# Kernel tuning notes

Measured on AMD Instinct MI355X. Metric: run time of the kernel, lower is better.

The kernel has to match this reference:

```python
import jax, jax.numpy as jnp
import numpy as np

N = 50000
E = 800000


def _segment_softmax(logits, seg, n):
    m = jax.ops.segment_max(logits, seg, num_segments=n)
    e = jnp.exp(logits - m[seg])
    s = jax.ops.segment_sum(e, seg, num_segments=n)
    return e / (s[seg] + 1e-16)


def _gin_layer(x, src, dst, w1, b1, w2, b2, n):
    # GINConv, eps=0: mlp(x + sum_{j->i} x_j); MLP = Linear-ReLU-Linear
    agg = jax.ops.segment_sum(x[src], dst, num_segments=n)
    h = x + agg
    h = jnp.maximum(h @ w1 + b1, 0.0)
    return h @ w2 + b2


def _gat_layer(x, src, dst, w, a_src, a_dst, b, n):
    # GATConv heads=1, add_self_loops=True, leaky_relu slope 0.2
    src = jnp.concatenate([src, jnp.arange(n, dtype=src.dtype)])
    dst = jnp.concatenate([dst, jnp.arange(n, dtype=dst.dtype)])
    h = x @ w                                  # [N, D]
    alpha_s = h @ a_src                        # [N]
    alpha_d = h @ a_dst                        # [N]
    logits = jax.nn.leaky_relu(alpha_s[src] + alpha_d[dst], negative_slope=0.2)
    alpha = _segment_softmax(logits, dst, n)   # [E+N]
    out = jax.ops.segment_sum(h[src] * alpha[:, None], dst, num_segments=n)
    return out + b


def setup_inputs() -> dict:
    key = jax.random.key(0)
    ks = jax.random.split(key, 24)

    def w(k, shape, fan_in):
        return (jax.random.normal(k, shape, dtype=jnp.float32) * (1.0 / np.sqrt(fan_in))).astype(jnp.float32)

    inp = {
        "x": jax.random.normal(ks[0], (N, 10), dtype=jnp.float32),
        "edge_index": jax.random.randint(ks[1], (2, E), 0, N, dtype=jnp.int64 if jax.config.jax_enable_x64 else jnp.int32),
        "edge_attr": jax.random.normal(ks[2], (E, 3), dtype=jnp.float32),
        # GIN layer 1: MLP([10, 64, 64])
        "gin1_w1": w(ks[3], (10, 64), 10), "gin1_b1": jnp.zeros((64,), jnp.float32),
        "gin1_w2": w(ks[4], (64, 64), 64), "gin1_b2": jnp.zeros((64,), jnp.float32),
        # GIN layer 2: MLP([64, 128, 128])
        "gin2_w1": w(ks[5], (64, 128), 64), "gin2_b1": jnp.zeros((128,), jnp.float32),
        "gin2_w2": w(ks[6], (128, 128), 128), "gin2_b2": jnp.zeros((128,), jnp.float32),
        # GAT layer 1: 128 -> 256, heads=1
        "gat1_w": w(ks[7], (128, 256), 128),
        "gat1_asrc": w(ks[8], (256,), 256), "gat1_adst": w(ks[9], (256,), 256),
        "gat1_b": jnp.zeros((256,), jnp.float32),
        # GAT layer 2: 256 -> 128, heads=1, concat=False
        "gat2_w": w(ks[10], (256, 128), 256),
        "gat2_asrc": w(ks[11], (128,), 128), "gat2_adst": w(ks[12], (128,), 128),
        "gat2_b": jnp.zeros((128,), jnp.float32),
    }
    return inp


def reference(x, edge_index, edge_attr,
              gin1_w1, gin1_b1, gin1_w2, gin1_b2,
              gin2_w1, gin2_b1, gin2_w2, gin2_b2,
              gat1_w, gat1_asrc, gat1_adst, gat1_b,
              gat2_w, gat2_asrc, gat2_adst, gat2_b):
    src, dst = edge_index[0], edge_index[1]
    n = x.shape[0]
    # edge_attr is accepted but ignored (GINConv does not consume edge features)
    h = _gin_layer(x, src, dst, gin1_w1, gin1_b1, gin1_w2, gin1_b2, n)
    h = jnp.maximum(h, 0.0)
    h = _gin_layer(h, src, dst, gin2_w1, gin2_b1, gin2_w2, gin2_b2, n)
    h = _gat_layer(h, src, dst, gat1_w, gat1_asrc, gat1_adst, gat1_b, n)
    h = jnp.maximum(h, 0.0)
    h = _gat_layer(h, src, dst, gat2_w, gat2_asrc, gat2_adst, gat2_b, n)
    return h
```

## Files before the change

kernel.cpp:

```cpp
#include <hip/hip_runtime.h>
#include <math.h>

__device__ __forceinline__ float lrelu(float x){ return x > 0.f ? x : 0.2f*x; }

typedef short s16x8 __attribute__((ext_vector_type(8)));
typedef float f32x4 __attribute__((ext_vector_type(4)));
typedef unsigned short u16x8 __attribute__((ext_vector_type(8)));

__device__ __forceinline__ f32x4 bmma(s16x8 a, s16x8 b, f32x4 c){
  return __builtin_amdgcn_mfma_f32_16x16x32_bf16(a, b, c, 0, 0, 0);
}

__device__ __forceinline__ unsigned short f2bf(float f){
  unsigned u = __float_as_uint(f);
  unsigned r = (u + 0x7fffu + ((u >> 16) & 1u)) >> 16;
  return (unsigned short)r;
}
__device__ __forceinline__ float bf2f(unsigned short h){
  return __uint_as_float(((unsigned)h) << 16);
}

__global__ void k_deg(const int* __restrict__ dst, int* __restrict__ deg, int E){
  int e = blockIdx.x*blockDim.x + threadIdx.x;
  if(e < E) atomicAdd(&deg[dst[e]], 1);
}

__global__ __launch_bounds__(1024) void k_scan1(const int* __restrict__ deg,
                                                int* __restrict__ part,
                                                int* __restrict__ bsum, int n){
  int i = blockIdx.x*1024 + threadIdx.x;
  int lane = threadIdx.x & 63, wv = threadIdx.x >> 6;
  int v = (i < n) ? deg[i] : 0;
  int s = v;
  #pragma unroll
  for(int off=1; off<64; off<<=1){
    int t = __shfl_up(s, off);
    if(lane >= off) s += t;
  }
  __shared__ int wsum[16];
  if(lane==63) wsum[wv] = s;
  __syncthreads();
  if(wv==0 && lane<16){
    int t = wsum[lane], ss = t;
    #pragma unroll
    for(int off=1; off<16; off<<=1){
      int u = __shfl_up(ss, off);
      if(lane >= off) ss += u;
    }
    wsum[lane] = ss - t;
    if(lane==15) bsum[blockIdx.x] = ss;
  }
  __syncthreads();
  if(i < n) part[i] = s - v + wsum[wv];
}

__global__ __launch_bounds__(1024) void k_scan2(int* __restrict__ bsum, int nb){
  int i = threadIdx.x;
  int lane = i & 63, wv = i >> 6;
  int v = (i < nb) ? bsum[i] : 0;
  int s = v;
  #pragma unroll
  for(int off=1; off<64; off<<=1){
    int t = __shfl_up(s, off);
    if(lane >= off) s += t;
  }
  __shared__ int wsum[16];
  if(lane==63) wsum[wv] = s;
  __syncthreads();
  if(wv==0 && lane<16){
    int t = wsum[lane], ss = t;
    #pragma unroll
    for(int off=1; off<16; off<<=1){
      int u = __shfl_up(ss, off);
      if(lane >= off) ss += u;
    }
    wsum[lane] = ss - t;
  }
  __syncthreads();
  if(i < nb) bsum[i] = s - v + wsum[wv];
}

__global__ void k_scan3(const int* __restrict__ part, const int* __restrict__ bsum,
                        int* __restrict__ offs, int n, int E){
  int i = blockIdx.x*blockDim.x + threadIdx.x;
  if(i < n) offs[i] = part[i] + bsum[i >> 10];
  if(i == 0) offs[n] = E;
}

__global__ void k_fill(const int* __restrict__ src, const int* __restrict__ dst,
                       const int* __restrict__ offs, int* __restrict__ cur,
                       int* __restrict__ esrc, int E){
  int e = blockIdx.x*blockDim.x + threadIdx.x;
  if(e < E){
    int d = dst[e];
    int pos = offs[d] + atomicAdd(&cur[d], 1);
    esrc[pos] = src[e];
  }
}

template<int D>
__global__ __launch_bounds__(256) void k_agg(const float* __restrict__ xin,
                                             const int* __restrict__ offs,
                                             const int* __restrict__ esrc,
                                             float* __restrict__ out, int n){
  int wid  = (int)((blockIdx.x*256u + threadIdx.x) >> 6);
  int lane = threadIdx.x & 63;
  if(wid >= n) return;
  constexpr int NC = (D + 63) / 64;
  float acc[NC];
  #pragma unroll
  for(int j=0;j<NC;j++){ int c = lane + j*64; acc[j] = (c<D) ? xin[(size_t)wid*D + c] : 0.f; }
  int e0 = offs[wid], e1 = offs[wid+1];
  for(int t=e0; t<e1; t++){
    int s = esrc[t];
    const float* row = xin + (size_t)s*D;
    #pragma unroll
    for(int j=0;j<NC;j++){ int c = lane + j*64; if(c<D) acc[j] += row[c]; }
  }
  #pragma unroll
  for(int j=0;j<NC;j++){ int c = lane + j*64; if(c<D) out[(size_t)wid*D + c] = acc[j]; }
}

__global__ __launch_bounds__(256) void k_gin2_agg(const unsigned short* __restrict__ xin,
                                                  const int* __restrict__ offs,
                                                  const int* __restrict__ esrc,
                                                  unsigned short* __restrict__ fhi,
                                                  unsigned short* __restrict__ flo, int n){
  int wid  = (int)((blockIdx.x*256u + threadIdx.x) >> 6);
  int lane = threadIdx.x & 63;
  if(wid >= n) return;
  int g = lane >> 3, sub = lane & 7;
  float acc[8];
  #pragma unroll
  for(int k=0;k<8;k++) acc[k] = 0.f;
  int e0 = offs[wid], e1 = offs[wid+1];
  int t = e0;
  for(; t+7 < e1; t += 8){
    int s = esrc[t + g];
    u16x8 r = *(const u16x8*)(xin + (size_t)s*64 + 8*sub);
    #pragma unroll
    for(int k=0;k<8;k++) acc[k] += bf2f(r[k]);
  }
  if(t < e1){
    int idx = t + g;
    bool ok = idx < e1;
    int s = esrc[ok ? idx : e0];
    u16x8 r = *(const u16x8*)(xin + (size_t)s*64 + 8*sub);
    float w = ok ? 1.f : 0.f;
    #pragma unroll
    for(int k=0;k<8;k++) acc[k] += w*bf2f(r[k]);
  }
  #pragma unroll
  for(int off=32; off>=8; off>>=1)
    #pragma unroll
    for(int k=0;k<8;k++) acc[k] += __shfl_down(acc[k], off);
  if(lane < 8){
    u16x8 rs = *(const u16x8*)(xin + (size_t)wid*64 + 8*sub);
    u16x8 h, l;
    #pragma unroll
    for(int k=0;k<8;k++){
      float o = acc[k] + bf2f(rs[k]);
      unsigned short hb = f2bf(o);
      h[k] = hb; l[k] = f2bf(o - bf2f(hb));
    }
    int mc = wid >> 4;
    size_t base = ((size_t)(mc*2 + (sub>>2))*64 + (wid & 15) + (sub & 3)*16) * 8;
    *(u16x8*)(fhi + base) = h;
    *(u16x8*)(flo + base) = l;
  }
}

__global__ __launch_bounds__(256) void k_prepA(const float* __restrict__ A,
                                               unsigned short* __restrict__ hi,
                                               unsigned short* __restrict__ lo,
                                               int M, int K, int Mc, int Kc){
  int gid = blockIdx.x*256 + threadIdx.x;
  int lane = gid & 63;
  int fid  = gid >> 6;
  if(fid >= Mc*Kc) return;
  int mc = fid / Kc, kc = fid - mc*Kc;
  int row = mc*16 + (lane & 15);
  int k0  = kc*32 + (lane >> 4)*8;
  s16x8 h, l;
  if(row < M){
    const float* ap = A + (size_t)row*K + k0;
    #pragma unroll
    for(int j=0;j<8;j++){
      float v = (k0 + j < K) ? ap[j] : 0.f;
      unsigned short hb = f2bf(v);
      float r = v - bf2f(hb);
      h[j] = (short)hb; l[j] = (short)f2bf(r);
    }
  } else {
    #pragma unroll
    for(int j=0;j<8;j++){ h[j]=0; l[j]=0; }
  }
  size_t off = (size_t)fid*512 + (size_t)lane*8;
  *(s16x8*)(hi + off) = h;
  *(s16x8*)(lo + off) = l;
}

__global__ __launch_bounds__(256) void k_prepB(const float* __restrict__ B,
                                               unsigned short* __restrict__ hi,
                                               unsigned short* __restrict__ lo,
                                               int K, int Nd, int Kc, int Nc){
  int gid = blockIdx.x*256 + threadIdx.x;
  int lane = gid & 63;
  int fid  = gid >> 6;
  if(fid >= Nc*Kc) return;
  int nc = fid / Kc, kc = fid - nc*Kc;
  int col = nc*16 + (lane & 15);
  int k0  = kc*32 + (lane >> 4)*8;
  s16x8 h, l;
  #pragma unroll
  for(int j=0;j<8;j++){
    int k = k0 + j;
    float v = (k < K) ? B[(size_t)k*Nd + col] : 0.f;
    unsigned short hb = f2bf(v);
    float r = v - bf2f(hb);
    h[j] = (short)hb; l[j] = (short)f2bf(r);
  }
  size_t off = (size_t)fid*512 + (size_t)lane*8;
  *(s16x8*)(hi + off) = h;
  *(s16x8*)(lo + off) = l;
}

template<int ACT, bool HASBIAS, int OMODE>
__global__ __launch_bounds__(256) void k_mgemm(const unsigned short* __restrict__ Ahi,
                                               const unsigned short* __restrict__ Alo,
                                               const unsigned short* __restrict__ Bhi,
                                               const unsigned short* __restrict__ Blo,
                                               const float* __restrict__ bias,
                                               float* __restrict__ C,
                                               unsigned short* __restrict__ Cbf,
                                               unsigned short* __restrict__ foh,
                                               unsigned short* __restrict__ fol,
                                               const float* __restrict__ dwS,
                                               const float* __restrict__ dwD,
                                               float* __restrict__ dotS,
                                               float* __restrict__ dotD,
                                               int M, int Nd, int Kc, int Mc){
  int tid = threadIdx.x;
  int wid = tid >> 6, lane = tid & 63;
  int wm = wid >> 1, wn = wid & 1;
  int mcb = blockIdx.x*8 + wm*4;
  int ncb = blockIdx.y*4 + wn*2;

  f32x4 acc[4][2];
  #pragma unroll
  for(int f=0;f<4;f++)
    #pragma unroll
    for(int g=0;g<2;g++) acc[f][g] = (f32x4){0.f,0.f,0.f,0.f};

  for(int kc=0; kc<Kc; kc++){
    s16x8 ah[4], al[4], bh[2], bl[2];
    #pragma unroll
    for(int f=0;f<4;f++){
      int mcf = mcb + f; if(mcf > Mc-1) mcf = Mc-1;
      size_t off = ((size_t)mcf*Kc + kc)*512 + (size_t)lane*8;
      ah[f] = *(const s16x8*)(Ahi + off);
      al[f] = *(const s16x8*)(Alo + off);
    }
    #pragma unroll
    for(int g=0;g<2;g++){
      size_t off = ((size_t)(ncb+g)*Kc + kc)*512 + (size_t)lane*8;
      bh[g] = *(const s16x8*)(Bhi + off);
      bl[g] = *(const s16x8*)(Blo + off);
    }
    #pragma unroll
    for(int f=0;f<4;f++)
      #pragma unroll
      for(int g=0;g<2;g++){
        acc[f][g] = bmma(ah[f], bh[g], acc[f][g]);
        acc[f][g] = bmma(ah[f], bl[g], acc[f][g]);
        acc[f][g] = bmma(al[f], bh[g], acc[f][g]);
      }
  }

  if constexpr(OMODE <= 1){
    #pragma unroll
    for(int g=0;g<2;g++){
      int col = (ncb+g)*16 + (lane & 15);
      float bv = HASBIAS ? bias[col] : 0.f;
      #pragma unroll
      for(int f=0;f<4;f++){
        int row0 = (mcb+f)*16 + (lane>>4)*4;
        #pragma unroll
        for(int r=0;r<4;r++){
          int row = row0 + r;
          if(row < M){
            float v = acc[f][g][r] + bv;
            if(ACT) v = fmaxf(v, 0.f);
            if(OMODE==1) Cbf[(size_t)row*Nd + col] = f2bf(v);
            else         C  [(size_t)row*Nd + col] = v;
          }
        }
      }
    }
  } else {
    __shared__ float tile[4][64][33];
    #pragma unroll
    for(int g=0;g<2;g++){
      float bv = HASBIAS ? bias[(ncb+g)*16 + (lane&15)] : 0.f;
      int ck = g*16 + (lane & 15);
      #pragma unroll
      for(int f=0;f<4;f++){
        int rb = f*16 + (lane>>4)*4;
        #pragma unroll
        for(int r=0;r<4;r++){
          float v = acc[f][g][r] + bv;
          if(ACT) v = fmaxf(v, 0.f);
          tile[wid][rb + r][ck] = v;
        }
      }
    }
    asm volatile("" ::: "memory");
    int Kcn = Nd >> 5;
    int kcn = ncb >> 1;
    int rr = lane & 15, cb = lane >> 4;
    #pragma unroll
    for(int f=0;f<4;f++){
      int mcf = mcb + f;
      if(mcf >= Mc) continue;
      float o[8];
      #pragma unroll
      for(int j=0;j<8;j++) o[j] = tile[wid][f*16 + rr][cb*8 + j];
      if constexpr(OMODE == 4){
        u16x8 hb;
        #pragma unroll
        for(int j=0;j<8;j++) hb[j] = f2bf(o[j]);
        int row = mcf*16 + rr;
        *(u16x8*)(Cbf + (size_t)row*Nd + kcn*32 + cb*8) = hb;
      } else {
        u16x8 h, l;
        #pragma unroll
        for(int j=0;j<8;j++){
          unsigned short hb = f2bf(o[j]);
          h[j] = hb; l[j] = f2bf(o[j] - bf2f(hb));
        }
        size_t base = ((size_t)mcf*Kcn + kcn)*512 + (size_t)lane*8;
        *(u16x8*)(foh + base) = h;
        *(u16x8*)(fol + base) = l;
      }
      if constexpr(OMODE == 3 || OMODE == 4){
        float sv = 0.f, dv = 0.f;
        #pragma unroll
        for(int j=0;j<8;j++){
          int col = kcn*32 + cb*8 + j;
          sv += o[j]*dwS[col]; dv += o[j]*dwD[col];
        }
        sv += __shfl_xor(sv, 16); sv += __shfl_xor(sv, 32);
        dv += __shfl_xor(dv, 16); dv += __shfl_xor(dv, 32);
        if(cb == 0){
          int row = mcf*16 + rr;
          atomicAdd(dotS + row, sv);
          atomicAdd(dotD + row, dv);
        }
      }
    }
  }
}

template<int L>
__global__ __launch_bounds__(256) void k_wa(const float* __restrict__ W,
                                            const float* __restrict__ a_s, const float* __restrict__ a_d,
                                            float* __restrict__ wa_s, float* __restrict__ wa_d, int rows){
  int wid  = (int)((blockIdx.x*256u + threadIdx.x) >> 6);
  int lane = threadIdx.x & 63;
  if(wid >= rows) return;
  float s = 0.f, d = 0.f;
  #pragma unroll
  for(int j=0;j<L/64;j++){
    int c = lane + j*64;
    float v = W[(size_t)wid*L + c];
    s += v * a_s[c];
    d += v * a_d[c];
  }
  #pragma unroll
  for(int off=32; off; off>>=1){ s += __shfl_down(s, off); d += __shfl_down(d, off); }
  if(lane==0){ wa_s[wid] = s; wa_d[wid] = d; }
}

__global__ __launch_bounds__(256) void k_gat1_aggpre(const unsigned short* __restrict__ hB,
                                                     const float* __restrict__ as_, const float* __restrict__ ad_,
                                                     const int* __restrict__ offs, const int* __restrict__ esrc,
                                                     unsigned short* __restrict__ fhi, unsigned short* __restrict__ flo,
                                                     int n){
  int wid  = (int)((blockIdx.x*256u + threadIdx.x) >> 6);
  int lane = threadIdx.x & 63;
  if(wid >= n) return;
  int q = lane >> 4, sub = lane & 15;
  float adi = ad_[wid];
  u16x8 rs = *(const u16x8*)(hB + (size_t)wid*128 + 8*sub);
  float m, S, acc[8];
  if(q == 0){
    m = lrelu(as_[wid] + adi); S = 1.f;
    #pragma unroll
    for(int k=0;k<8;k++) acc[k] = bf2f(rs[k]);
  } else {
    m = -3e38f; S = 0.f;
    #pragma unroll
    for(int k=0;k<8;k++) acc[k] = 0.f;
  }
  int e0 = offs[wid], e1 = offs[wid+1];
  int t = e0;
  for(; t+7 < e1; t += 8){
    int s0 = esrc[t + q], s1 = esrc[t + 4 + q];
    u16x8 r0 = *(const u16x8*)(hB + (size_t)s0*128 + 8*sub);
    u16x8 r1 = *(const u16x8*)(hB + (size_t)s1*128 + 8*sub);
    float l0 = lrelu(as_[s0] + adi), l1 = lrelu(as_[s1] + adi);
    float lm = fmaxf(l0, l1);
    if(lm > m + 8.f){
      float sc = __expf(m - lm); S *= sc;
      #pragma unroll
      for(int k=0;k<8;k++) acc[k] *= sc;
      m = lm;
    }
    float w0 = __expf(l0 - m), w1 = __expf(l1 - m);
    S += w0 + w1;
    #pragma unroll
    for(int k=0;k<8;k++) acc[k] += w0*bf2f(r0[k]) + w1*bf2f(r1[k]);
  }
  while(t < e1){
    int idx = t + q;
    bool ok = idx < e1;
    int s = esrc[ok ? idx : e0];
    u16x8 r = *(const u16x8*)(hB + (size_t)s*128 + 8*sub);
    float l = ok ? lrelu(as_[s] + adi) : -3e38f;
    if(l > m + 8.f){
      float sc = __expf(m - l); S *= sc;
      #pragma unroll
      for(int k=0;k<8;k++) acc[k] *= sc;
      m = l;
    }
    float w = __expf(l - m);
    S += w;
    #pragma unroll
    for(int k=0;k<8;k++) acc[k] += w*bf2f(r[k]);
    t += 4;
  }
  #pragma unroll
  for(int off=32; off>=16; off>>=1){
    float mo = __shfl_down(m, off), So = __shfl_down(S, off);
    float ao[8];
    #pragma unroll
    for(int k=0;k<8;k++) ao[k] = __shfl_down(acc[k], off);
    float M = fmaxf(m, mo);
    float sc0 = __expf(m - M), sc1 = __expf(mo - M);
    S = S*sc0 + So*sc1;
    #pragma unroll
    for(int k=0;k<8;k++) acc[k] = acc[k]*sc0 + ao[k]*sc1;
    m = M;
  }
  if(lane < 16){
    float inv = 1.f/(S + 1e-16f);
    u16x8 h, l;
    #pragma unroll
    for(int k=0;k<8;k++){
      float v = acc[k]*inv;
      unsigned short hb = f2bf(v);
      h[k] = hb; l[k] = f2bf(v - bf2f(hb));
    }
    int mc = wid >> 4;
    size_t base = ((size_t)(mc*4 + (sub>>2))*64 + (wid & 15) + (sub & 3)*16) * 8;
    *(u16x8*)(fhi + base) = h;
    *(u16x8*)(flo + base) = l;
  }
}

__global__ __launch_bounds__(256) void k_gat2_agg(const unsigned short* __restrict__ hP,
                                                  const float* __restrict__ as_, const float* __restrict__ ad_,
                                                  const int* __restrict__ offs, const int* __restrict__ esrc,
                                                  const float* __restrict__ bias, float* __restrict__ out, int n){
  int wid  = (int)((blockIdx.x*256u + threadIdx.x) >> 6);
  int lane = threadIdx.x & 63;
  if(wid >= n) return;
  int q = lane >> 4, sub = lane & 15;
  float adi = ad_[wid];
  u16x8 rs = *(const u16x8*)(hP + (size_t)wid*128 + 8*sub);
  float m, S, acc[8];
  if(q == 0){
    m = lrelu(as_[wid] + adi); S = 1.f;
    #pragma unroll
    for(int k=0;k<8;k++) acc[k] = bf2f(rs[k]);
  } else {
    m = -3e38f; S = 0.f;
    #pragma unroll
    for(int k=0;k<8;k++) acc[k] = 0.f;
  }
  int e0 = offs[wid], e1 = offs[wid+1];
  int t = e0;
  for(; t+7 < e1; t += 8){
    int s0 = esrc[t + q], s1 = esrc[t + 4 + q];
    u16x8 r0 = *(const u16x8*)(hP + (size_t)s0*128 + 8*sub);
    u16x8 r1 = *(const u16x8*)(hP + (size_t)s1*128 + 8*sub);
    float l0 = lrelu(as_[s0] + adi), l1 = lrelu(as_[s1] + adi);
    float lm = fmaxf(l0, l1);
    if(lm > m + 8.f){
      float sc = __expf(m - lm); S *= sc;
      #pragma unroll
      for(int k=0;k<8;k++) acc[k] *= sc;
      m = lm;
    }
    float w0 = __expf(l0 - m), w1 = __expf(l1 - m);
    S += w0 + w1;
    #pragma unroll
    for(int k=0;k<8;k++) acc[k] += w0*bf2f(r0[k]) + w1*bf2f(r1[k]);
  }
  while(t < e1){
    int idx = t + q;
    bool ok = idx < e1;
    int s = esrc[ok ? idx : e0];
    u16x8 r = *(const u16x8*)(hP + (size_t)s*128 + 8*sub);
    float l = ok ? lrelu(as_[s] + adi) : -3e38f;
    if(l > m + 8.f){
      float sc = __expf(m - l); S *= sc;
      #pragma unroll
      for(int k=0;k<8;k++) acc[k] *= sc;
      m = l;
    }
    float w = __expf(l - m);
    S += w;
    #pragma unroll
    for(int k=0;k<8;k++) acc[k] += w*bf2f(r[k]);
    t += 4;
  }
  #pragma unroll
  for(int off=32; off>=16; off>>=1){
    float mo = __shfl_down(m, off), So = __shfl_down(S, off);
    float ao[8];
    #pragma unroll
    for(int k=0;k<8;k++) ao[k] = __shfl_down(acc[k], off);
    float M = fmaxf(m, mo);
    float sc0 = __expf(m - M), sc1 = __expf(mo - M);
    S = S*sc0 + So*sc1;
    #pragma unroll
    for(int k=0;k<8;k++) acc[k] = acc[k]*sc0 + ao[k]*sc1;
    m = M;
  }
  if(lane < 16){
    float inv = 1.f/(S + 1e-16f);
    float4 o0, o1;
    o0.x = acc[0]*inv + bias[8*sub  ]; o0.y = acc[1]*inv + bias[8*sub+1];
    o0.z = acc[2]*inv + bias[8*sub+2]; o0.w = acc[3]*inv + bias[8*sub+3];
    o1.x = acc[4]*inv + bias[8*sub+4]; o1.y = acc[5]*inv + bias[8*sub+5];
    o1.z = acc[6]*inv + bias[8*sub+6]; o1.w = acc[7]*inv + bias[8*sub+7];
    *(float4*)(out + (size_t)wid*128 + 8*sub)     = o0;
    *(float4*)(out + (size_t)wid*128 + 8*sub + 4) = o1;
  }
}

extern "C" void kernel_launch(void* const* d_in, const int* in_sizes, int n_in,
                              void* d_out, int out_size, void* d_ws, size_t ws_size,
                              hipStream_t stream){
  const float* x        = (const float*)d_in[0];
  const int*   ei       = (const int*)  d_in[1];
  const float* gin1_w1  = (const float*)d_in[3];
  const float* gin1_b1  = (const float*)d_in[4];
  const float* gin1_w2  = (const float*)d_in[5];
  const float* gin1_b2  = (const float*)d_in[6];
  const float* gin2_w1  = (const float*)d_in[7];
  const float* gin2_b1  = (const float*)d_in[8];
  const float* gin2_w2  = (const float*)d_in[9];
  const float* gin2_b2  = (const float*)d_in[10];
  const float* gat1_w   = (const float*)d_in[11];
  const float* gat1_as  = (const float*)d_in[12];
  const float* gat1_ad  = (const float*)d_in[13];
  const float* gat1_b   = (const float*)d_in[14];
  const float* gat2_w   = (const float*)d_in[15];
  const float* gat2_as  = (const float*)d_in[16];
  const float* gat2_ad  = (const float*)d_in[17];
  const float* gat2_b   = (const float*)d_in[18];

  const int n = in_sizes[0] / 10;
  const int E = in_sizes[1] / 2;
  const int* src = ei;
  const int* dst = ei + E;
  const int Mc = (n + 15) / 16;
  const int nb = (n + 1023) / 1024;

  char* w = (char*)d_ws;
  auto carve = [&](size_t bytes)->char*{ char* p = w; w += (bytes + 255) & ~(size_t)255; return p; };
  int*   esrc = (int*)  carve((size_t)E*4);
  int*   offs = (int*)  carve((size_t)(n+1)*4);
  int*   deg  = (int*)  carve((size_t)n*4);
  int*   cur  = (int*)  carve((size_t)n*4);
  int*   part = (int*)  carve((size_t)n*4);
  int*   bsum = (int*)  carve((size_t)1024*4);
  float* F1   = (float*)carve((size_t)n*16*4);
  unsigned short* Hbf   = (unsigned short*)carve((size_t)n*64*2);
  unsigned short* hB2bf = (unsigned short*)carve((size_t)n*128*2);
  unsigned short* Pbf2  = (unsigned short*)carve((size_t)n*128*2);
  float* as_  = (float*)carve((size_t)n*4);
  float* ad_  = (float*)carve((size_t)n*4);
  float* as2_ = (float*)carve((size_t)n*4);
  float* ad2_ = (float*)carve((size_t)n*4);
  float* waS  = (float*)carve(256*4);
  float* waD  = (float*)carve(256*4);
  float* waS2 = (float*)carve(256*4);
  float* waD2 = (float*)carve(256*4);
  unsigned short* FAh = (unsigned short*)carve((size_t)Mc*8*512*2);
  unsigned short* FAl = (unsigned short*)carve((size_t)Mc*8*512*2);
  unsigned short* FBh = (unsigned short*)carve((size_t)Mc*8*512*2);
  unsigned short* FBl = (unsigned short*)carve((size_t)Mc*8*512*2);
  unsigned short* BfH = (unsigned short*)carve((size_t)64*512*2);
  unsigned short* BfL = (unsigned short*)carve((size_t)64*512*2);

  const int TPB = 256;
  int ebk = (E + TPB - 1) / TPB;
  int wbk = (n + 3) / 4;
  int gx  = (Mc + 7) / 8;

  hipMemsetAsync(deg, 0, (size_t)n*4, stream);
  hipMemsetAsync(cur, 0, (size_t)n*4, stream);
  k_deg<<<ebk, TPB, 0, stream>>>(dst, deg, E);
  k_scan1<<<nb, 1024, 0, stream>>>(deg, part, bsum, n);
  k_scan2<<<1, 1024, 0, stream>>>(bsum, nb);
  k_scan3<<<(n + 1023)/1024, 1024, 0, stream>>>(part, bsum, offs, n, E);
  k_fill<<<ebk, TPB, 0, stream>>>(src, dst, offs, cur, esrc, E);

  k_wa<256><<<(128+3)/4, TPB, 0, stream>>>(gat1_w, gat1_as, gat1_ad, waS, waD, 128);
  k_wa<128><<<(256+3)/4, TPB, 0, stream>>>(gat2_w, gat2_as, gat2_ad, waS2, waD2, 256);

  k_agg<10><<<wbk, TPB, 0, stream>>>(x, offs, esrc, F1, n);
  k_prepA<<<(Mc*1*64 + 255)/256, 256, 0, stream>>>(F1, FAh, FAl, n, 10, Mc, 1);
  k_prepB<<<(4*1*64 + 255)/256, 256, 0, stream>>>(gin1_w1, BfH, BfL, 10, 64, 1, 4);
  k_mgemm<1,true,2><<<dim3(gx,1), TPB, 0, stream>>>(FAh, FAl, BfH, BfL, gin1_b1,
      nullptr, nullptr, FBh, FBl, nullptr, nullptr, nullptr, nullptr, n, 64, 1, Mc);
  k_prepB<<<(4*2*64 + 255)/256, 256, 0, stream>>>(gin1_w2, BfH, BfL, 64, 64, 2, 4);
  k_mgemm<1,true,1><<<dim3(gx,1), TPB, 0, stream>>>(FBh, FBl, BfH, BfL, gin1_b2,
      nullptr, Hbf, nullptr, nullptr, nullptr, nullptr, nullptr, nullptr, n, 64, 2, Mc);

  k_gin2_agg<<<wbk, TPB, 0, stream>>>(Hbf, offs, esrc, FAh, FAl, n);
  k_prepB<<<(8*2*64 + 255)/256, 256, 0, stream>>>(gin2_w1, BfH, BfL, 64, 128, 2, 8);
  k_mgemm<1,true,2><<<dim3(gx,2), TPB, 0, stream>>>(FAh, FAl, BfH, BfL, gin2_b1,
      nullptr, nullptr, FBh, FBl, nullptr, nullptr, nullptr, nullptr, n, 128, 2, Mc);
  hipMemsetAsync(as_, 0, (size_t)n*4, stream);
  hipMemsetAsync(ad_, 0, (size_t)n*4, stream);
  k_prepB<<<(8*4*64 + 255)/256, 256, 0, stream>>>(gin2_w2, BfH, BfL, 128, 128, 4, 8);
  k_mgemm<0,true,4><<<dim3(gx,2), TPB, 0, stream>>>(FBh, FBl, BfH, BfL, gin2_b2,
      nullptr, hB2bf, nullptr, nullptr, waS, waD, as_, ad_, n, 128, 4, Mc);

  k_gat1_aggpre<<<wbk, TPB, 0, stream>>>(hB2bf, as_, ad_, offs, esrc, FAh, FAl, n);
  hipMemsetAsync(as2_, 0, (size_t)n*4, stream);
  hipMemsetAsync(ad2_, 0, (size_t)n*4, stream);
  k_prepB<<<(16*4*64 + 255)/256, 256, 0, stream>>>(gat1_w, BfH, BfL, 128, 256, 4, 16);
  k_mgemm<1,true,3><<<dim3(gx,4), TPB, 0, stream>>>(FAh, FAl, BfH, BfL, gat1_b,
      nullptr, nullptr, FBh, FBl, waS2, waD2, as2_, ad2_, n, 256, 4, Mc);

  k_prepB<<<(8*8*64 + 255)/256, 256, 0, stream>>>(gat2_w, BfH, BfL, 256, 128, 8, 8);
  k_mgemm<0,false,1><<<dim3(gx,2), TPB, 0, stream>>>(FBh, FBl, BfH, BfL, nullptr,
      nullptr, Pbf2, nullptr, nullptr, nullptr, nullptr, nullptr, nullptr, n, 128, 8, Mc);
  k_gat2_agg<<<wbk, TPB, 0, stream>>>(Pbf2, as2_, ad2_, offs, esrc, gat2_b, (float*)d_out, n);
}
```

Before: 376.2 us.

## Reorder GIN1 as transform-then-aggregate and fold memsets into scan kernel

GIN layer 1 now multiplies x by W1 first and aggregates the 64-wide bf16 result, using linearity of the sum. Bias and ReLU move into the aggregation kernel, which replaces the separate fp32 10-wide aggregation and its prep step. The four attention-score memsets are folded into k_scan3, and the deg/cur memsets are merged into a single contiguous memset. This trades a narrow fp32 gather for a wider bf16 gather, and the bf16 rounding of W1·x happens before the sum, which can change numerics slightly.

```diff
diff --git a/kernel.cpp b/kernel.cpp
--- a/kernel.cpp
+++ b/kernel.cpp
@@ -81,9 +81,15 @@
 }
 
 __global__ void k_scan3(const int* __restrict__ part, const int* __restrict__ bsum,
-                        int* __restrict__ offs, int n, int E){
+                        int* __restrict__ offs,
+                        float* __restrict__ z0, float* __restrict__ z1,
+                        float* __restrict__ z2, float* __restrict__ z3,
+                        int n, int E){
   int i = blockIdx.x*blockDim.x + threadIdx.x;
-  if(i < n) offs[i] = part[i] + bsum[i >> 10];
+  if(i < n){
+    offs[i] = part[i] + bsum[i >> 10];
+    z0[i] = 0.f; z1[i] = 0.f; z2[i] = 0.f; z3[i] = 0.f;
+  }
   if(i == 0) offs[n] = E;
 }
 
@@ -98,34 +104,13 @@
   }
 }
 
-template<int D>
-__global__ __launch_bounds__(256) void k_agg(const float* __restrict__ xin,
-                                             const int* __restrict__ offs,
-                                             const int* __restrict__ esrc,
-                                             float* __restrict__ out, int n){
-  int wid  = (int)((blockIdx.x*256u + threadIdx.x) >> 6);
-  int lane = threadIdx.x & 63;
-  if(wid >= n) return;
-  constexpr int NC = (D + 63) / 64;
-  float acc[NC];
-  #pragma unroll
-  for(int j=0;j<NC;j++){ int c = lane + j*64; acc[j] = (c<D) ? xin[(size_t)wid*D + c] : 0.f; }
-  int e0 = offs[wid], e1 = offs[wid+1];
-  for(int t=e0; t<e1; t++){
-    int s = esrc[t];
-    const float* row = xin + (size_t)s*D;
-    #pragma unroll
-    for(int j=0;j<NC;j++){ int c = lane + j*64; if(c<D) acc[j] += row[c]; }
-  }
-  #pragma unroll
-  for(int j=0;j<NC;j++){ int c = lane + j*64; if(c<D) out[(size_t)wid*D + c] = acc[j]; }
-}
-
-__global__ __launch_bounds__(256) void k_gin2_agg(const unsigned short* __restrict__ xin,
-                                                  const int* __restrict__ offs,
-                                                  const int* __restrict__ esrc,
-                                                  unsigned short* __restrict__ fhi,
-                                                  unsigned short* __restrict__ flo, int n){
+template<bool BR>
+__global__ __launch_bounds__(256) void k_gin_agg(const unsigned short* __restrict__ xin,
+                                                 const int* __restrict__ offs,
+                                                 const int* __restrict__ esrc,
+                                                 const float* __restrict__ bias,
+                                                 unsigned short* __restrict__ fhi,
+                                                 unsigned short* __restrict__ flo, int n){
   int wid  = (int)((blockIdx.x*256u + threadIdx.x) >> 6);
   int lane = threadIdx.x & 63;
   if(wid >= n) return;
@@ -160,6 +145,7 @@
     #pragma unroll
     for(int k=0;k<8;k++){
       float o = acc[k] + bf2f(rs[k]);
+      if(BR) o = fmaxf(o + bias[8*sub + k], 0.f);
       unsigned short hb = f2bf(o);
       h[k] = hb; l[k] = f2bf(o - bf2f(hb));
     }
@@ -578,16 +564,17 @@
   const int* dst = ei + E;
   const int Mc = (n + 15) / 16;
   const int nb = (n + 1023) / 1024;
+  const size_t npad = ((size_t)n*4 + 255) & ~(size_t)255;
 
   char* w = (char*)d_ws;
   auto carve = [&](size_t bytes)->char*{ char* p = w; w += (bytes + 255) & ~(size_t)255; return p; };
   int*   esrc = (int*)  carve((size_t)E*4);
   int*   offs = (int*)  carve((size_t)(n+1)*4);
-  int*   deg  = (int*)  carve((size_t)n*4);
-  int*   cur  = (int*)  carve((size_t)n*4);
+  int*   deg  = (int*)  carve(npad);
+  int*   cur  = (int*)  carve(npad);
   int*   part = (int*)  carve((size_t)n*4);
   int*   bsum = (int*)  carve((size_t)1024*4);
-  float* F1   = (float*)carve((size_t)n*16*4);
+  unsigned short* Ybf   = (unsigned short*)carve((size_t)n*64*2);
   unsigned short* Hbf   = (unsigned short*)carve((size_t)n*64*2);
   unsigned short* hB2bf = (unsigned short*)carve((size_t)n*128*2);
   unsigned short* Pbf2  = (unsigned short*)carve((size_t)n*128*2);
@@ -611,39 +598,34 @@
   int wbk = (n + 3) / 4;
   int gx  = (Mc + 7) / 8;
 
-  hipMemsetAsync(deg, 0, (size_t)n*4, stream);
-  hipMemsetAsync(cur, 0, (size_t)n*4, stream);
+  hipMemsetAsync(deg, 0, npad*2, stream);
   k_deg<<<ebk, TPB, 0, stream>>>(dst, deg, E);
   k_scan1<<<nb, 1024, 0, stream>>>(deg, part, bsum, n);
   k_scan2<<<1, 1024, 0, stream>>>(bsum, nb);
-  k_scan3<<<(n + 1023)/1024, 1024, 0, stream>>>(part, bsum, offs, n, E);
+  k_scan3<<<(n + 1023)/1024, 1024, 0, stream>>>(part, bsum, offs, as_, ad_, as2_, ad2_, n, E);
   k_fill<<<ebk, TPB, 0, stream>>>(src, dst, offs, cur, esrc, E);
 
   k_wa<256><<<(128+3)/4, TPB, 0, stream>>>(gat1_w, gat1_as, gat1_ad, waS, waD, 128);
   k_wa<128><<<(256+3)/4, TPB, 0, stream>>>(gat2_w, gat2_as, gat2_ad, waS2, waD2, 256);
 
-  k_agg<10><<<wbk, TPB, 0, stream>>>(x, offs, esrc, F1, n);
-  k_prepA<<<(Mc*1*64 + 255)/256, 256, 0, stream>>>(F1, FAh, FAl, n, 10, Mc, 1);
+  k_prepA<<<(Mc*1*64 + 255)/256, 256, 0, stream>>>(x, FAh, FAl, n, 10, Mc, 1);
   k_prepB<<<(4*1*64 + 255)/256, 256, 0, stream>>>(gin1_w1, BfH, BfL, 10, 64, 1, 4);
-  k_mgemm<1,true,2><<<dim3(gx,1), TPB, 0, stream>>>(FAh, FAl, BfH, BfL, gin1_b1,
-      nullptr, nullptr, FBh, FBl, nullptr, nullptr, nullptr, nullptr, n, 64, 1, Mc);
+  k_mgemm<0,false,1><<<dim3(gx,1), TPB, 0, stream>>>(FAh, FAl, BfH, BfL, nullptr,
+      nullptr, Ybf, nullptr, nullptr, nullptr, nullptr, nullptr, nullptr, n, 64, 1, Mc);
+  k_gin_agg<true><<<wbk, TPB, 0, stream>>>(Ybf, offs, esrc, gin1_b1, FBh, FBl, n);
   k_prepB<<<(4*2*64 + 255)/256, 256, 0, stream>>>(gin1_w2, BfH, BfL, 64, 64, 2, 4);
   k_mgemm<1,true,1><<<dim3(gx,1), TPB, 0, stream>>>(FBh, FBl, BfH, BfL, gin1_b2,
       nullptr, Hbf, nullptr, nullptr, nullptr, nullptr, nullptr, nullptr, n, 64, 2, Mc);
 
-  k_gin2_agg<<<wbk, TPB, 0, stream>>>(Hbf, offs, esrc, FAh, FAl, n);
+  k_gin_agg<false><<<wbk, TPB, 0, stream>>>(Hbf, offs, esrc, nullptr, FAh, FAl, n);
   k_prepB<<<(8*2*64 + 255)/256, 256, 0, stream>>>(gin2_w1, BfH, BfL, 64, 128, 2, 8);
   k_mgemm<1,true,2><<<dim3(gx,2), TPB, 0, stream>>>(FAh, FAl, BfH, BfL, gin2_b1,
       nullptr, nullptr, FBh, FBl, nullptr, nullptr, nullptr, nullptr, n, 128, 2, Mc);
-  hipMemsetAsync(as_, 0, (size_t)n*4, stream);
-  hipMemsetAsync(ad_, 0, (size_t)n*4, stream);
   k_prepB<<<(8*4*64 + 255)/256, 256, 0, stream>>>(gin2_w2, BfH, BfL, 128, 128, 4, 8);
   k_mgemm<0,true,4><<<dim3(gx,2), TPB, 0, stream>>>(FBh, FBl, BfH, BfL, gin2_b2,
       nullptr, hB2bf, nullptr, nullptr, waS, waD, as_, ad_, n, 128, 4, Mc);
 
   k_gat1_aggpre<<<wbk, TPB, 0, stream>>>(hB2bf, as_, ad_, offs, esrc, FAh, FAl, n);
-  hipMemsetAsync(as2_, 0, (size_t)n*4, stream);
-  hipMemsetAsync(ad2_, 0, (size_t)n*4, stream);
   k_prepB<<<(16*4*64 + 255)/256, 256, 0, stream>>>(gat1_w, BfH, BfL, 128, 256, 4, 16);
   k_mgemm<1,true,3><<<dim3(gx,4), TPB, 0, stream>>>(FAh, FAl, BfH, BfL, gat1_b,
       nullptr, nullptr, FBh, FBl, waS2, waD2, as2_, ad2_, n, 256, 4, Mc);
```

After: 343.2 us. -8.8%, faster.
